# Optimization experiments

Hardware: AMD Instinct MI355X
Metric: run time of the kernel (lower is better)

## Reference

```python
import jax, jax.numpy as jnp
import numpy as np

T, B, E, H, L, V = 35, 128, 200, 512, 2, 10000


def setup_inputs() -> dict:
    key = jax.random.key(0)
    ks = jax.random.split(key, 8)
    s = 0.05  # weight init scale
    return {
        "inputs": jax.random.randint(ks[0], (T, B), 0, V),
        "hidden": jnp.zeros((L, B, H), jnp.float32),
        "emb": jax.random.normal(ks[1], (V, E), jnp.float32) * s,
        "Wx0": jax.random.normal(ks[2], (3, H, E), jnp.float32) * s,
        "Wx": jax.random.normal(ks[3], (L - 1, 3, H, H), jnp.float32) * s,
        "Wh": jax.random.normal(ks[4], (L, 3, H, H), jnp.float32) * s,
        "bh": jax.random.normal(ks[5], (L, 3, H), jnp.float32) * s,
        "Wout": jax.random.normal(ks[6], (V, H), jnp.float32) * s,
        "bout": jnp.zeros((V,), jnp.float32),
    }


def reference(inputs, hidden, emb, Wx0, Wx, Wh, bh, Wout, bout):
    # inputs: [T,B] int; hidden: [L,B,H]
    x = emb[inputs]  # [T,B,E]
    num_layers = hidden.shape[0]

    def step(h_prev, x_t):
        data = x_t  # dropout is identity (keep_prob=1.0)
        new_h = []
        for j in range(num_layers):
            Wxj = Wx0 if j == 0 else Wx[j - 1]
            gx = jnp.einsum('bi,ghi->gbh', data, Wxj)  # [3,B,H], no bias on x-side
            hp = h_prev[j]
            reset = jax.nn.sigmoid(gx[0] + hp @ Wh[j, 0].T + bh[j, 0])
            forget = jax.nn.sigmoid(gx[1] + hp @ Wh[j, 1].T + bh[j, 1])
            tild = jnp.tanh(gx[2] + (reset * hp) @ Wh[j, 2].T + bh[j, 2])
            hn = (1.0 - forget) * hp + forget * tild
            new_h.append(hn)
            data = hn  # dropout identity
        logit = data @ Wout.T + bout  # [B,V]
        return jnp.stack(new_h), logit

    h_final, logits = jax.lax.scan(step, hidden, x)
    return logits, h_final
```

## Files before the change

kernel.cpp:

```cpp
#include <hip/hip_runtime.h>
#include <hip/hip_bf16.h>

#define T_ 35
#define B_ 128
#define E_ 200
#define H_ 512
#define L_ 2
#define V_ 10000
#define BH_ (B_ * H_)
#define KPAD 224
#define NCL 4
#define CLW 48
#define NWG (NCL * CLW)

typedef __attribute__((ext_vector_type(8))) short bf16x8;
typedef __attribute__((ext_vector_type(4))) float f32x4;

__device__ __forceinline__ unsigned short f2bf(float f) {
    union { float f; unsigned u; } c; c.f = f;
    unsigned r = c.u + 0x7FFF + ((c.u >> 16) & 1);
    return (unsigned short)(r >> 16);
}
__device__ __forceinline__ float bf2f(unsigned short u) {
    union { unsigned u; float f; } c; c.u = ((unsigned)u) << 16; return c.f;
}

__device__ __forceinline__ bf16x8 cvt8(const float* src) {
    float4 w0 = *(const float4*)src;
    float4 w1 = *(const float4*)(src + 4);
    bf16x8 v;
    v[0] = (short)f2bf(w0.x); v[1] = (short)f2bf(w0.y);
    v[2] = (short)f2bf(w0.z); v[3] = (short)f2bf(w0.w);
    v[4] = (short)f2bf(w1.x); v[5] = (short)f2bf(w1.y);
    v[6] = (short)f2bf(w1.z); v[7] = (short)f2bf(w1.w);
    return v;
}

__device__ __forceinline__ void store_quad_bf16(unsigned short* buf, int idx,
                                                float v, int lane) {
    unsigned x = (unsigned)f2bf(v);
    unsigned y = (unsigned)__shfl_xor((int)x, 1);
    unsigned pair = (lane & 1) ? (y | (x << 16)) : (x | (y << 16));
    unsigned long long q = (unsigned long long)pair;
    unsigned long long p2 = (unsigned long long)(unsigned)__shfl_xor((int)pair, 2);
    unsigned long long quad = (lane & 2) ? (p2 | (q << 32)) : (q | (p2 << 32));
    if ((lane & 3) == 0)
        __hip_atomic_store((unsigned long long*)(buf + idx), quad,
                           __ATOMIC_RELAXED, __HIP_MEMORY_SCOPE_AGENT);
}

__global__ void prep_all(const float* __restrict__ emb, const float* __restrict__ Wx0,
                         const float* __restrict__ hidden, const float* __restrict__ Wout,
                         unsigned short* embB, unsigned short* wx0cat,
                         unsigned short* WoutB,
                         unsigned short* h0bt, unsigned short* h1bfx, int* flags) {
    int job = blockIdx.y;
    int stride = gridDim.x * blockDim.x;
    int i0 = blockIdx.x * blockDim.x + threadIdx.x;
    if (job == 0) {
        for (int i = i0; i < V_ * KPAD; i += stride) {
            int v = i / KPAD, k = i - v * KPAD;
            embB[i] = (k < E_) ? f2bf(emb[v * E_ + k]) : (unsigned short)0;
        }
    } else if (job == 1) {
        for (int i = i0; i < 1536 * KPAD; i += stride) {
            int n = i / KPAD, k = i - n * KPAD;
            wx0cat[i] = (k < E_) ? f2bf(Wx0[n * E_ + k]) : (unsigned short)0;
        }
    } else if (job == 2) {
        for (int i = i0; i < 2 * BH_; i += stride) {
            if (i < BH_) h0bt[i] = f2bf(hidden[i]);
            else         h1bfx[i - BH_] = f2bf(hidden[i]);
        }
        for (int i = i0; i < NWG * 32; i += stride) flags[i] = 0;
    } else {
        for (int i = i0; i < V_ * H_; i += stride) WoutB[i] = f2bf(Wout[i]);
    }
}

__global__ __launch_bounds__(256) void xside_gemm(
    const int* __restrict__ inputs, const unsigned short* __restrict__ embB,
    const unsigned short* __restrict__ wx0cat, float* __restrict__ gx0) {
    int m0 = blockIdx.x * 128, n0 = blockIdx.y * 128;
    int wave = threadIdx.x >> 6, lane = threadIdx.x & 63;
    int wr = wave >> 1, wc = wave & 1;
    int am = m0 + wr * 64, bn = n0 + wc * 64;
    int lr = lane & 15, lk = (lane >> 4) * 8;

    f32x4 acc[4][4] = {};
    int id[4];
    #pragma unroll
    for (int i = 0; i < 4; ++i) id[i] = inputs[am + i * 16 + lr];

    for (int k0 = 0; k0 < KPAD; k0 += 32) {
        bf16x8 a[4], b[4];
        #pragma unroll
        for (int i = 0; i < 4; ++i)
            a[i] = *(const bf16x8*)(embB + (size_t)id[i] * KPAD + k0 + lk);
        #pragma unroll
        for (int j = 0; j < 4; ++j)
            b[j] = *(const bf16x8*)(wx0cat + (size_t)(bn + j * 16 + lr) * KPAD + k0 + lk);
        #pragma unroll
        for (int i = 0; i < 4; ++i)
            #pragma unroll
            for (int j = 0; j < 4; ++j)
                acc[i][j] = __builtin_amdgcn_mfma_f32_16x16x32_bf16(a[i], b[j], acc[i][j], 0, 0, 0);
    }
    int crow0 = (lane >> 4) * 4, ccol = lane & 15;
    #pragma unroll
    for (int i = 0; i < 4; ++i) {
        #pragma unroll
        for (int r = 0; r < 4; ++r) {
            int row = am + i * 16 + crow0 + r;
            int t = row >> 7, b = row & 127;
            #pragma unroll
            for (int j = 0; j < 4; ++j) {
                int col = bn + j * 16 + ccol;
                int g = col >> 9, h = col & 511;
                gx0[((size_t)(t * 3 + g) * 128 + b) * 512 + h] = acc[i][j][r];
            }
        }
    }
}

__device__ __forceinline__ void bar_l0(int* flb, int wgl, int gen) {
    __syncthreads();
    if (threadIdx.x == 0)
        __hip_atomic_store(flb + wgl * 32, gen,
                           __ATOMIC_RELAXED, __HIP_MEMORY_SCOPE_AGENT);
    if (threadIdx.x < 16) {
        while (__hip_atomic_load(flb + threadIdx.x * 32, __ATOMIC_RELAXED,
                                 __HIP_MEMORY_SCOPE_AGENT) < gen)
            __builtin_amdgcn_s_sleep(1);
    }
    __syncthreads();
}

__device__ __forceinline__ void bar_l1(int* flb, int wid, int gen, int l0need) {
    __syncthreads();
    if (threadIdx.x == 0)
        __hip_atomic_store(flb + (16 + wid) * 32, gen,
                           __ATOMIC_RELAXED, __HIP_MEMORY_SCOPE_AGENT);
    if (threadIdx.x < 32) {
        while (__hip_atomic_load(flb + (16 + threadIdx.x) * 32, __ATOMIC_RELAXED,
                                 __HIP_MEMORY_SCOPE_AGENT) < gen)
            __builtin_amdgcn_s_sleep(1);
    } else if (threadIdx.x < 48) {
        while (__hip_atomic_load(flb + (threadIdx.x - 32) * 32, __ATOMIC_RELAXED,
                                 __HIP_MEMORY_SCOPE_AGENT) < l0need)
            __builtin_amdgcn_s_sleep(1);
    }
    __syncthreads();
}

__global__ __launch_bounds__(512) void scan_kernel(
    const float* __restrict__ gx0,
    const float* __restrict__ Wx, const float* __restrict__ Wh,
    const float* __restrict__ bh, const float* __restrict__ hidden,
    unsigned short* h0bt, unsigned short* rh0t, unsigned short* rh1t,
    unsigned short* h1bfx, int* flags, float* hfinal_out) {
    __shared__ unsigned short wlds[96 * 512];

    const int tid = threadIdx.x;
    const int bx = blockIdx.x;
    const int cl = bx & 3;
    const int wgl = bx >> 2;
    const int lane = tid & 63;
    const int wave = tid >> 6;
    const int lr = lane & 15;
    const int hi = lane >> 4;
    const int lk8 = hi * 8;
    const int ccol = lane & 15;
    const int crow0 = hi * 4;
    const int R0 = cl * 32;

    const bool isL0 = (wgl < 16);
    const int wid = wgl - 16;
    int* flb = flags + cl * CLW * 32;

    if (isL0) {
        for (int i = tid; i < 96 * 64; i += 512) {
            int lc = i >> 6, kg = i & 63;
            int g = lc >> 5, h = (wgl << 5) + (lc & 31);
            const float* src = Wh + (size_t)(g * 512 + h) * 512 + kg * 8;
            *(bf16x8*)(wlds + lc * 512 + (kg ^ (lc & 7)) * 8) = cvt8(src);
        }
    } else {
        for (int i = tid; i < 48 * 128; i += 512) {
            int lc = i >> 7, kg = i & 127;
            int g = lc >> 4, h = (wid << 4) + (lc & 15);
            const float* src = (kg < 64)
                ? Wx + (size_t)(g * 512 + h) * 512 + kg * 8
                : Wh + (size_t)(3 * 512 * 512) + (size_t)(g * 512 + h) * 512 + (kg - 64) * 8;
            *(bf16x8*)(wlds + lc * 1024 + (kg ^ (lc & 7)) * 8) = cvt8(src);
        }
    }

    const int mt0 = wave >> 2, nt0 = wave & 3;
    const int mt1 = (wave >> 1) & 1, nt1 = wave & 1;
    float h0reg[4], freg0[4], bias_p1_0 = 0.f, bias_p2_0 = 0.f;
    float h1reg[4], freg1[4], bias_p1_1 = 0.f, bias_p2_1 = 0.f;
    bf16x8 a0keep[16];

    if (isL0) {
        const int base = wgl << 5;
        int g = nt0 >> 1;
        int hp1 = base + (nt0 & 1) * 16 + ccol;
        bias_p1_0 = bh[g * 512 + hp1];
        if (nt0 >= 2) {
            int hc = base + (nt0 - 2) * 16 + ccol;
            int rowg = R0 + mt0 * 16;
            #pragma unroll
            for (int r = 0; r < 4; ++r)
                h0reg[r] = hidden[(size_t)(rowg + crow0 + r) * 512 + hc];
            bias_p2_0 = bh[1024 + hc];
        }
    } else {
        const int base = wid << 4;
        int hc = base + ccol;
        if (wave < 4) {
            bias_p1_1 = bh[1536 + nt1 * 512 + hc];
            if (nt1 == 1) {
                int rowg = R0 + mt1 * 16;
                #pragma unroll
                for (int r = 0; r < 4; ++r)
                    h1reg[r] = hidden[(size_t)BH_ + (size_t)(rowg + crow0 + r) * 512 + hc];
                bias_p2_1 = bh[2560 + hc];
            }
        }
    }
    __syncthreads();

    if (isL0) {
        const int base = wgl << 5;
        const int rowg = R0 + mt0 * 16;
        const int hP1 = base + (nt0 & 1) * 16 + ccol;
        const int gP1 = nt0 >> 1;
        const int ntp = (nt0 >= 2) ? (nt0 - 2) : 0;
        const int hP2 = base + ntp * 16 + ccol;

        float gxn[4];
        {
            const float* gx = gx0 + (size_t)(0 * 3 + gP1) * BH_ + hP1;
            #pragma unroll
            for (int r = 0; r < 4; ++r)
                gxn[r] = gx[(rowg + crow0 + r) * 512];
        }

        for (int s = 0; s < 2 * T_; ++s) {
            bar_l0(flb, wgl, s);
            int t = s >> 1;
            float gxc[4];
            #pragma unroll
            for (int r = 0; r < 4; ++r) gxc[r] = gxn[r];
            if (s + 1 < 2 * T_) {
                int tn = (s + 1) >> 1;
                const float* gx = (((s + 1) & 1) == 0)
                    ? gx0 + (size_t)(tn * 3 + gP1) * BH_ + hP1
                    : gx0 + (size_t)(tn * 3 + 2) * BH_ + hP2;
                #pragma unroll
                for (int r = 0; r < 4; ++r)
                    gxn[r] = gx[(rowg + crow0 + r) * 512];
            }
            if ((s & 1) == 0) {
                const unsigned short* hprev = h0bt + (size_t)t * BH_;
                unsigned short* rh0 = rh0t + (size_t)t * BH_;
                bf16x8 a[16];
                #pragma unroll
                for (int ks = 0; ks < 16; ++ks)
                    a[ks] = *(const bf16x8*)(hprev + (size_t)(rowg + lr) * 512 + ks * 32 + lk8);
                f32x4 accA = {0.f, 0.f, 0.f, 0.f}, accB = {0.f, 0.f, 0.f, 0.f};
                #pragma unroll
                for (int ks = 0; ks < 16; ks += 2) {
                    int c = nt0 * 16 + lr;
                    int kgA = 4 * ks + hi, kgB = 4 * (ks + 1) + hi;
                    bf16x8 bA = *(const bf16x8*)(wlds + c * 512 + (kgA ^ (c & 7)) * 8);
                    bf16x8 bB = *(const bf16x8*)(wlds + c * 512 + (kgB ^ (c & 7)) * 8);
                    accA = __builtin_amdgcn_mfma_f32_16x16x32_bf16(a[ks], bA, accA, 0, 0, 0);
                    accB = __builtin_amdgcn_mfma_f32_16x16x32_bf16(a[ks + 1], bB, accB, 0, 0, 0);
                }
                #pragma unroll
                for (int r = 0; r < 4; ++r) {
                    int b = rowg + crow0 + r;
                    float v = accA[r] + accB[r] + gxc[r] + bias_p1_0;
                    float sg = 1.f / (1.f + __expf(-v));
                    if (nt0 < 2) {
                        float h0p = bf2f(hprev[(size_t)b * 512 + hP1]);
                        store_quad_bf16(rh0, b * 512 + hP1 - (lane & 3), sg * h0p, lane);
                    } else {
                        freg0[r] = sg;
                    }
                }
            } else if (nt0 >= 2) {
                const unsigned short* rh0 = rh0t + (size_t)t * BH_;
                unsigned short* h0nx = h0bt + (size_t)(t + 1) * BH_;
                bf16x8 a[16];
                #pragma unroll
                for (int ks = 0; ks < 16; ++ks)
                    a[ks] = *(const bf16x8*)(rh0 + (size_t)(rowg + lr) * 512 + ks * 32 + lk8);
                f32x4 accA = {0.f, 0.f, 0.f, 0.f}, accB = {0.f, 0.f, 0.f, 0.f};
                #pragma unroll
                for (int ks = 0; ks < 16; ks += 2) {
                    int c = 64 + ntp * 16 + lr;
                    int kgA = 4 * ks + hi, kgB = 4 * (ks + 1) + hi;
                    bf16x8 bA = *(const bf16x8*)(wlds + c * 512 + (kgA ^ (c & 7)) * 8);
                    bf16x8 bB = *(const bf16x8*)(wlds + c * 512 + (kgB ^ (c & 7)) * 8);
                    accA = __builtin_amdgcn_mfma_f32_16x16x32_bf16(a[ks], bA, accA, 0, 0, 0);
                    accB = __builtin_amdgcn_mfma_f32_16x16x32_bf16(a[ks + 1], bB, accB, 0, 0, 0);
                }
                #pragma unroll
                for (int r = 0; r < 4; ++r) {
                    int b = rowg + crow0 + r;
                    float v = accA[r] + accB[r] + gxc[r] + bias_p2_0;
                    float tld = tanhf(v);
                    float hn = h0reg[r] + freg0[r] * (tld - h0reg[r]);
                    h0reg[r] = hn;
                    store_quad_bf16(h0nx, b * 512 + hP2 - (lane & 3), hn, lane);
                }
            }
        }
        __syncthreads();
        if (tid == 0)
            __hip_atomic_store(flb + wgl * 32, 2 * T_,
                               __ATOMIC_RELAXED, __HIP_MEMORY_SCOPE_AGENT);
        if (nt0 >= 2) {
            #pragma unroll
            for (int r = 0; r < 4; ++r)
                hfinal_out[(size_t)(rowg + crow0 + r) * 512 + hP2] = h0reg[r];
        }
    } else {
        for (int s = 0; s < 2 * T_; ++s) {
            int tc = s >> 1;
            int l0need = ((s & 1) == 0) ? (2 * tc + 2) : 0;
            bar_l1(flb, wid, s, l0need);
            if ((s & 1) == 0) {
                if (wave < 4) {
                    const int base = wid << 4;
                    const int rowg = R0 + mt1 * 16;
                    const unsigned short* h0cur = h0bt + (size_t)(tc + 1) * BH_;
                    const unsigned short* h1prev = h1bfx + (size_t)tc * BH_;
                    unsigned short* rh1 = rh1t + (size_t)tc * BH_;
                    bf16x8 a1[16];
                    #pragma unroll
                    for (int ks = 0; ks < 16; ++ks) {
                        a0keep[ks] = *(const bf16x8*)(h0cur + (size_t)(rowg + lr) * 512 + ks * 32 + lk8);
                        a1[ks] = *(const bf16x8*)(h1prev + (size_t)(rowg + lr) * 512 + ks * 32 + lk8);
                    }
                    f32x4 accA = {0.f, 0.f, 0.f, 0.f}, accB = {0.f, 0.f, 0.f, 0.f};
                    #pragma unroll
                    for (int ks = 0; ks < 16; ++ks) {
                        int kg = 4 * ks + hi;
                        int c = nt1 * 16 + lr;
                        bf16x8 b = *(const bf16x8*)(wlds + c * 1024 + (kg ^ (c & 7)) * 8);
                        accA = __builtin_amdgcn_mfma_f32_16x16x32_bf16(a0keep[ks], b, accA, 0, 0, 0);
                    }
                    #pragma unroll
                    for (int ks = 0; ks < 16; ++ks) {
                        int kg = 64 + 4 * ks + hi;
                        int c = nt1 * 16 + lr;
                        bf16x8 b = *(const bf16x8*)(wlds + c * 1024 + (kg ^ (c & 7)) * 8);
                        accB = __builtin_amdgcn_mfma_f32_16x16x32_bf16(a1[ks], b, accB, 0, 0, 0);
                    }
                    int h = base + ccol;
                    #pragma unroll
                    for (int r = 0; r < 4; ++r) {
                        int b = rowg + crow0 + r;
                        float v = accA[r] + accB[r] + bias_p1_1;
                        float sg = 1.f / (1.f + __expf(-v));
                        if (nt1 == 0) {
                            float h1p = bf2f(h1prev[(size_t)b * 512 + h]);
                            store_quad_bf16(rh1, b * 512 + h - (lane & 3), sg * h1p, lane);
                        } else {
                            freg1[r] = sg;
                        }
                    }
                }
            } else {
                if (wave < 4 && nt1 == 1) {
                    const int base = wid << 4;
                    const int rowg = R0 + mt1 * 16;
                    const unsigned short* rh1 = rh1t + (size_t)tc * BH_;
                    unsigned short* h1nx = h1bfx + (size_t)(tc + 1) * BH_;
                    bf16x8 a1[16];
                    #pragma unroll
                    for (int ks = 0; ks < 16; ++ks)
                        a1[ks] = *(const bf16x8*)(rh1 + (size_t)(rowg + lr) * 512 + ks * 32 + lk8);
                    f32x4 accA = {0.f, 0.f, 0.f, 0.f}, accB = {0.f, 0.f, 0.f, 0.f};
                    #pragma unroll
                    for (int ks = 0; ks < 16; ++ks) {
                        int kg = 4 * ks + hi;
                        int c = 32 + lr;
                        bf16x8 b = *(const bf16x8*)(wlds + c * 1024 + (kg ^ (c & 7)) * 8);
                        accA = __builtin_amdgcn_mfma_f32_16x16x32_bf16(a0keep[ks], b, accA, 0, 0, 0);
                    }
                    #pragma unroll
                    for (int ks = 0; ks < 16; ++ks) {
                        int kg = 64 + 4 * ks + hi;
                        int c = 32 + lr;
                        bf16x8 b = *(const bf16x8*)(wlds + c * 1024 + (kg ^ (c & 7)) * 8);
                        accB = __builtin_amdgcn_mfma_f32_16x16x32_bf16(a1[ks], b, accB, 0, 0, 0);
                    }
                    int h = base + ccol;
                    #pragma unroll
                    for (int r = 0; r < 4; ++r) {
                        int b = rowg + crow0 + r;
                        float v = accA[r] + accB[r] + bias_p2_1;
                        float tld = tanhf(v);
                        float hn = h1reg[r] + freg1[r] * (tld - h1reg[r]);
                        h1reg[r] = hn;
                        store_quad_bf16(h1nx, b * 512 + h - (lane & 3), hn, lane);
                    }
                }
            }
        }
        if (wave < 4 && nt1 == 1) {
            const int base = wid << 4;
            int rowg = R0 + mt1 * 16;
            #pragma unroll
            for (int r = 0; r < 4; ++r)
                hfinal_out[(size_t)BH_ + (size_t)(rowg + crow0 + r) * 512 + base + ccol] = h1reg[r];
        }
    }
}

#define MT_ (T_ * B_ / 128)
#define NT_ ((V_ + 127) / 128)
__global__ __launch_bounds__(256) void logits_gemm(
    const unsigned short* __restrict__ A, const unsigned short* __restrict__ Bw,
    const float* __restrict__ bout, float* __restrict__ C) {
    const int nwg = MT_ * NT_;
    const int q = nwg / 8, rr = nwg % 8;
    int bid = blockIdx.x;
    int xcd = bid % 8, idx = bid / 8;
    int wgid = (xcd < rr ? xcd * (q + 1) : rr * (q + 1) + (xcd - rr) * q) + idx;
    int n0 = (wgid / MT_) * 128;
    int m0 = (wgid % MT_) * 128;

    int wave = threadIdx.x >> 6, lane = threadIdx.x & 63;
    int wr = wave >> 1, wc = wave & 1;
    int am = m0 + wr * 64, bn = n0 + wc * 64;
    int lr = lane & 15, lk = (lane >> 4) * 8;

    f32x4 acc[4][4] = {};
    bf16x8 a[4], b[4], an[4], bnx[4];
    #pragma unroll
    for (int i = 0; i < 4; ++i)
        a[i] = *(const bf16x8*)(A + (size_t)(am + i * 16 + lr) * H_ + lk);
    #pragma unroll
    for (int j = 0; j < 4; ++j) {
        int colc = bn + j * 16 + lr; if (colc >= V_) colc = V_ - 1;
        b[j] = *(const bf16x8*)(Bw + (size_t)colc * H_ + lk);
    }
    for (int k0 = 0; k0 < H_; k0 += 32) {
        if (k0 + 32 < H_) {
            #pragma unroll
            for (int i = 0; i < 4; ++i)
                an[i] = *(const bf16x8*)(A + (size_t)(am + i * 16 + lr) * H_ + k0 + 32 + lk);
            #pragma unroll
            for (int j = 0; j < 4; ++j) {
                int colc = bn + j * 16 + lr; if (colc >= V_) colc = V_ - 1;
                bnx[j] = *(const bf16x8*)(Bw + (size_t)colc * H_ + k0 + 32 + lk);
            }
        }
        #pragma unroll
        for (int i = 0; i < 4; ++i)
            #pragma unroll
            for (int j = 0; j < 4; ++j)
                acc[i][j] = __builtin_amdgcn_mfma_f32_16x16x32_bf16(a[i], b[j], acc[i][j], 0, 0, 0);
        #pragma unroll
        for (int i = 0; i < 4; ++i) { a[i] = an[i]; b[i] = bnx[i]; }
    }
    int crow0 = (lane >> 4) * 4, ccol = lane & 15;
    #pragma unroll
    for (int j = 0; j < 4; ++j) {
        int col = bn + j * 16 + ccol;
        if (col >= V_) continue;
        float bv = bout[col];
        #pragma unroll
        for (int i = 0; i < 4; ++i) {
            #pragma unroll
            for (int r = 0; r < 4; ++r) {
                int row = am + i * 16 + crow0 + r;
                __builtin_nontemporal_store(acc[i][j][r] + bv, &C[(size_t)row * V_ + col]);
            }
        }
    }
}

extern "C" void kernel_launch(void* const* d_in, const int* in_sizes, int n_in,
                              void* d_out, int out_size, void* d_ws, size_t ws_size,
                              hipStream_t stream) {
    const int*   inputs = (const int*)  d_in[0];
    const float* hidden = (const float*)d_in[1];
    const float* emb    = (const float*)d_in[2];
    const float* Wx0    = (const float*)d_in[3];
    const float* Wx     = (const float*)d_in[4];
    const float* Wh     = (const float*)d_in[5];
    const float* bh     = (const float*)d_in[6];
    const float* Wout   = (const float*)d_in[7];
    const float* bout   = (const float*)d_in[8];
    float* out = (float*)d_out;
    (void)in_sizes; (void)n_in; (void)out_size; (void)ws_size;

    char* ws = (char*)d_ws;
    size_t off = 0;
    auto alloc = [&](size_t bytes) -> void* {
        void* p = ws + off;
        off += (bytes + 255) & ~(size_t)255;
        return p;
    };
    unsigned short* embB   = (unsigned short*)alloc((size_t)V_ * KPAD * 2);
    unsigned short* wx0cat = (unsigned short*)alloc((size_t)1536 * KPAD * 2);
    unsigned short* WoutB  = (unsigned short*)alloc((size_t)V_ * H_ * 2);
    unsigned short* h1bfx  = (unsigned short*)alloc((size_t)(T_ + 1) * BH_ * 2);
    int* flags = (int*)alloc(NWG * 32 * 4);

    float* gx0 = out;
    unsigned short* scr = (unsigned short*)(out + (size_t)T_ * 3 * BH_);
    unsigned short* h0bt = scr;
    unsigned short* rh0t = scr + (size_t)(T_ + 1) * BH_;
    unsigned short* rh1t = scr + (size_t)(2 * T_ + 1) * BH_;

    prep_all<<<dim3(1024, 4), dim3(256), 0, stream>>>(
        emb, Wx0, hidden, Wout, embB, wx0cat, WoutB, h0bt, h1bfx, flags);
    xside_gemm<<<dim3(T_, 12), dim3(256), 0, stream>>>(inputs, embB, wx0cat, gx0);
    scan_kernel<<<dim3(NWG), dim3(512), 0, stream>>>(
        gx0, Wx, Wh, bh, hidden,
        h0bt, rh0t, rh1t, h1bfx, flags,
        out + (size_t)T_ * B_ * V_);
    logits_gemm<<<dim3(MT_ * NT_), dim3(256), 0, stream>>>(
        h1bfx + BH_, WoutB, bout, out);
}
```

Measured before the change: 595.1 us.

## Fuse logits GEMM into persistent scan kernel with atomic tile queue

Merges the recurrent scan and the output-projection GEMM into one persistent launch. Extra workgroups, and the scan workgroups once they finish, pull logits tiles from an atomic queue. Each tile spin-waits on per-cluster layer-1 progress flags, so logits for a time step can start as soon as that step's hidden state exists, overlapping the GEMM with the serial scan. Tiles whose output rows alias the gx0 and scratch buffers are deferred until the scan completes. The cost is memory and compute contention on the latency-bound scan, plus smaller 128x128 tiles and extra polling.

```diff
diff --git a/kernel.cpp b/kernel.cpp
--- a/kernel.cpp
+++ b/kernel.cpp
@@ -12,6 +12,9 @@
 #define NCL 4
 #define CLW 48
 #define NWG (NCL * CLW)
+#define TOTWG 256
+#define NTL 79
+#define NTILES (T_ * NTL)
 
 typedef __attribute__((ext_vector_type(8))) short bf16x8;
 typedef __attribute__((ext_vector_type(4))) float f32x4;
@@ -72,7 +75,7 @@
             if (i < BH_) h0bt[i] = f2bf(hidden[i]);
             else         h1bfx[i - BH_] = f2bf(hidden[i]);
         }
-        for (int i = i0; i < NWG * 32; i += stride) flags[i] = 0;
+        for (int i = i0; i < NWG * 32 + 32; i += stride) flags[i] = 0;
     } else {
         for (int i = i0; i < V_ * H_; i += stride) WoutB[i] = f2bf(Wout[i]);
     }
@@ -153,18 +156,19 @@
     __syncthreads();
 }
 
-__global__ __launch_bounds__(512) void scan_kernel(
+__global__ __launch_bounds__(512) void scan_logits_kernel(
     const float* __restrict__ gx0,
     const float* __restrict__ Wx, const float* __restrict__ Wh,
     const float* __restrict__ bh, const float* __restrict__ hidden,
     unsigned short* h0bt, unsigned short* rh0t, unsigned short* rh1t,
-    unsigned short* h1bfx, int* flags, float* hfinal_out) {
+    unsigned short* h1bfx, int* flags,
+    const unsigned short* __restrict__ WoutB, const float* __restrict__ bout,
+    float* __restrict__ C, float* hfinal_out) {
     __shared__ unsigned short wlds[96 * 512];
+    __shared__ int qidx_sh;
 
     const int tid = threadIdx.x;
     const int bx = blockIdx.x;
-    const int cl = bx & 3;
-    const int wgl = bx >> 2;
     const int lane = tid & 63;
     const int wave = tid >> 6;
     const int lr = lane & 15;
@@ -172,316 +176,335 @@
     const int lk8 = hi * 8;
     const int ccol = lane & 15;
     const int crow0 = hi * 4;
-    const int R0 = cl * 32;
-
-    const bool isL0 = (wgl < 16);
-    const int wid = wgl - 16;
-    int* flb = flags + cl * CLW * 32;
-
-    if (isL0) {
-        for (int i = tid; i < 96 * 64; i += 512) {
-            int lc = i >> 6, kg = i & 63;
-            int g = lc >> 5, h = (wgl << 5) + (lc & 31);
-            const float* src = Wh + (size_t)(g * 512 + h) * 512 + kg * 8;
-            *(bf16x8*)(wlds + lc * 512 + (kg ^ (lc & 7)) * 8) = cvt8(src);
-        }
-    } else {
-        for (int i = tid; i < 48 * 128; i += 512) {
-            int lc = i >> 7, kg = i & 127;
-            int g = lc >> 4, h = (wid << 4) + (lc & 15);
-            const float* src = (kg < 64)
-                ? Wx + (size_t)(g * 512 + h) * 512 + kg * 8
-                : Wh + (size_t)(3 * 512 * 512) + (size_t)(g * 512 + h) * 512 + (kg - 64) * 8;
-            *(bf16x8*)(wlds + lc * 1024 + (kg ^ (lc & 7)) * 8) = cvt8(src);
-        }
-    }
-
-    const int mt0 = wave >> 2, nt0 = wave & 3;
-    const int mt1 = (wave >> 1) & 1, nt1 = wave & 1;
-    float h0reg[4], freg0[4], bias_p1_0 = 0.f, bias_p2_0 = 0.f;
-    float h1reg[4], freg1[4], bias_p1_1 = 0.f, bias_p2_1 = 0.f;
-    bf16x8 a0keep[16];
-
-    if (isL0) {
-        const int base = wgl << 5;
-        int g = nt0 >> 1;
-        int hp1 = base + (nt0 & 1) * 16 + ccol;
-        bias_p1_0 = bh[g * 512 + hp1];
-        if (nt0 >= 2) {
-            int hc = base + (nt0 - 2) * 16 + ccol;
-            int rowg = R0 + mt0 * 16;
-            #pragma unroll
-            for (int r = 0; r < 4; ++r)
-                h0reg[r] = hidden[(size_t)(rowg + crow0 + r) * 512 + hc];
-            bias_p2_0 = bh[1024 + hc];
-        }
-    } else {
-        const int base = wid << 4;
-        int hc = base + ccol;
-        if (wave < 4) {
-            bias_p1_1 = bh[1536 + nt1 * 512 + hc];
-            if (nt1 == 1) {
-                int rowg = R0 + mt1 * 16;
+    int* qhead = flags + NWG * 32;
+
+    if (bx < NWG) {
+        const int cl = bx & 3;
+        const int wgl = bx >> 2;
+        const int R0 = cl * 32;
+        const bool isL0 = (wgl < 16);
+        const int wid = wgl - 16;
+        int* flb = flags + cl * CLW * 32;
+
+        if (isL0) {
+            for (int i = tid; i < 96 * 64; i += 512) {
+                int lc = i >> 6, kg = i & 63;
+                int g = lc >> 5, h = (wgl << 5) + (lc & 31);
+                const float* src = Wh + (size_t)(g * 512 + h) * 512 + kg * 8;
+                *(bf16x8*)(wlds + lc * 512 + (kg ^ (lc & 7)) * 8) = cvt8(src);
+            }
+        } else {
+            for (int i = tid; i < 48 * 128; i += 512) {
+                int lc = i >> 7, kg = i & 127;
+                int g = lc >> 4, h = (wid << 4) + (lc & 15);
+                const float* src = (kg < 64)
+                    ? Wx + (size_t)(g * 512 + h) * 512 + kg * 8
+                    : Wh + (size_t)(3 * 512 * 512) + (size_t)(g * 512 + h) * 512 + (kg - 64) * 8;
+                *(bf16x8*)(wlds + lc * 1024 + (kg ^ (lc & 7)) * 8) = cvt8(src);
+            }
+        }
+
+        const int mt0 = wave >> 2, nt0 = wave & 3;
+        const int mt1 = (wave >> 1) & 1, nt1 = wave & 1;
+        float h0reg[4], freg0[4], bias_p1_0 = 0.f, bias_p2_0 = 0.f;
+        float h1reg[4], freg1[4], bias_p1_1 = 0.f, bias_p2_1 = 0.f;
+        bf16x8 a0keep[16];
+
+        if (isL0) {
+            const int base = wgl << 5;
+            int g = nt0 >> 1;
+            int hp1 = base + (nt0 & 1) * 16 + ccol;
+            bias_p1_0 = bh[g * 512 + hp1];
+            if (nt0 >= 2) {
+                int hc = base + (nt0 - 2) * 16 + ccol;
+                int rowg = R0 + mt0 * 16;
                 #pragma unroll
                 for (int r = 0; r < 4; ++r)
-                    h1reg[r] = hidden[(size_t)BH_ + (size_t)(rowg + crow0 + r) * 512 + hc];
-                bias_p2_1 = bh[2560 + hc];
-            }
-        }
-    }
-    __syncthreads();
-
-    if (isL0) {
-        const int base = wgl << 5;
-        const int rowg = R0 + mt0 * 16;
-        const int hP1 = base + (nt0 & 1) * 16 + ccol;
-        const int gP1 = nt0 >> 1;
-        const int ntp = (nt0 >= 2) ? (nt0 - 2) : 0;
-        const int hP2 = base + ntp * 16 + ccol;
-
-        float gxn[4];
-        {
-            const float* gx = gx0 + (size_t)(0 * 3 + gP1) * BH_ + hP1;
-            #pragma unroll
-            for (int r = 0; r < 4; ++r)
-                gxn[r] = gx[(rowg + crow0 + r) * 512];
-        }
-
-        for (int s = 0; s < 2 * T_; ++s) {
-            bar_l0(flb, wgl, s);
-            int t = s >> 1;
-            float gxc[4];
-            #pragma unroll
-            for (int r = 0; r < 4; ++r) gxc[r] = gxn[r];
-            if (s + 1 < 2 * T_) {
-                int tn = (s + 1) >> 1;
-                const float* gx = (((s + 1) & 1) == 0)
-                    ? gx0 + (size_t)(tn * 3 + gP1) * BH_ + hP1
-                    : gx0 + (size_t)(tn * 3 + 2) * BH_ + hP2;
+                    h0reg[r] = hidden[(size_t)(rowg + crow0 + r) * 512 + hc];
+                bias_p2_0 = bh[1024 + hc];
+            }
+        } else {
+            const int base = wid << 4;
+            int hc = base + ccol;
+            if (wave < 4) {
+                bias_p1_1 = bh[1536 + nt1 * 512 + hc];
+                if (nt1 == 1) {
+                    int rowg = R0 + mt1 * 16;
+                    #pragma unroll
+                    for (int r = 0; r < 4; ++r)
+                        h1reg[r] = hidden[(size_t)BH_ + (size_t)(rowg + crow0 + r) * 512 + hc];
+                    bias_p2_1 = bh[2560 + hc];
+                }
+            }
+        }
+        __syncthreads();
+
+        if (isL0) {
+            const int base = wgl << 5;
+            const int rowg = R0 + mt0 * 16;
+            const int hP1 = base + (nt0 & 1) * 16 + ccol;
+            const int gP1 = nt0 >> 1;
+            const int ntp = (nt0 >= 2) ? (nt0 - 2) : 0;
+            const int hP2 = base + ntp * 16 + ccol;
+
+            float gxn[4];
+            {
+                const float* gx = gx0 + (size_t)(0 * 3 + gP1) * BH_ + hP1;
                 #pragma unroll
                 for (int r = 0; r < 4; ++r)
                     gxn[r] = gx[(rowg + crow0 + r) * 512];
             }
-            if ((s & 1) == 0) {
-                const unsigned short* hprev = h0bt + (size_t)t * BH_;
-                unsigned short* rh0 = rh0t + (size_t)t * BH_;
-                bf16x8 a[16];
-                #pragma unroll
-                for (int ks = 0; ks < 16; ++ks)
-                    a[ks] = *(const bf16x8*)(hprev + (size_t)(rowg + lr) * 512 + ks * 32 + lk8);
-                f32x4 accA = {0.f, 0.f, 0.f, 0.f}, accB = {0.f, 0.f, 0.f, 0.f};
-                #pragma unroll
-                for (int ks = 0; ks < 16; ks += 2) {
-                    int c = nt0 * 16 + lr;
-                    int kgA = 4 * ks + hi, kgB = 4 * (ks + 1) + hi;
-                    bf16x8 bA = *(const bf16x8*)(wlds + c * 512 + (kgA ^ (c & 7)) * 8);
-                    bf16x8 bB = *(const bf16x8*)(wlds + c * 512 + (kgB ^ (c & 7)) * 8);
-                    accA = __builtin_amdgcn_mfma_f32_16x16x32_bf16(a[ks], bA, accA, 0, 0, 0);
-                    accB = __builtin_amdgcn_mfma_f32_16x16x32_bf16(a[ks + 1], bB, accB, 0, 0, 0);
+
+            for (int s = 0; s < 2 * T_; ++s) {
+                bar_l0(flb, wgl, s);
+                int t = s >> 1;
+                float gxc[4];
+                #pragma unroll
+                for (int r = 0; r < 4; ++r) gxc[r] = gxn[r];
+                if (s + 1 < 2 * T_) {
+                    int tn = (s + 1) >> 1;
+                    const float* gx = (((s + 1) & 1) == 0)
+                        ? gx0 + (size_t)(tn * 3 + gP1) * BH_ + hP1
+                        : gx0 + (size_t)(tn * 3 + 2) * BH_ + hP2;
+                    #pragma unroll
+                    for (int r = 0; r < 4; ++r)
+                        gxn[r] = gx[(rowg + crow0 + r) * 512];
                 }
-                #pragma unroll
-                for (int r = 0; r < 4; ++r) {
-                    int b = rowg + crow0 + r;
-                    float v = accA[r] + accB[r] + gxc[r] + bias_p1_0;
-                    float sg = 1.f / (1.f + __expf(-v));
-                    if (nt0 < 2) {
-                        float h0p = bf2f(hprev[(size_t)b * 512 + hP1]);
-                        store_quad_bf16(rh0, b * 512 + hP1 - (lane & 3), sg * h0p, lane);
-                    } else {
-                        freg0[r] = sg;
+                if ((s & 1) == 0) {
+                    const unsigned short* hprev = h0bt + (size_t)t * BH_;
+                    unsigned short* rh0 = rh0t + (size_t)t * BH_;
+                    bf16x8 a[16];
+                    #pragma unroll
+                    for (int ks = 0; ks < 16; ++ks)
+                        a[ks] = *(const bf16x8*)(hprev + (size_t)(rowg + lr) * 512 + ks * 32 + lk8);
+                    f32x4 accA = {0.f, 0.f, 0.f, 0.f}, accB = {0.f, 0.f, 0.f, 0.f};
+                    #pragma unroll
+                    for (int ks = 0; ks < 16; ks += 2) {
+                        int c = nt0 * 16 + lr;
+                        int kgA = 4 * ks + hi, kgB = 4 * (ks + 1) + hi;
+                        bf16x8 bA = *(const bf16x8*)(wlds + c * 512 + (kgA ^ (c & 7)) * 8);
+                        bf16x8 bB = *(const bf16x8*)(wlds + c * 512 + (kgB ^ (c & 7)) * 8);
+                        accA = __builtin_amdgcn_mfma_f32_16x16x32_bf16(a[ks], bA, accA, 0, 0, 0);
+                        accB = __builtin_amdgcn_mfma_f32_16x16x32_bf16(a[ks + 1], bB, accB, 0, 0, 0);
+                    }
+                    #pragma unroll
+                    for (int r = 0; r < 4; ++r) {
+                        int b = rowg + crow0 + r;
+                        float v = accA[r] + accB[r] + gxc[r] + bias_p1_0;
+                        float sg = 1.f / (1.f + __expf(-v));
+                        if (nt0 < 2) {
+                            float h0p = bf2f(hprev[(size_t)b * 512 + hP1]);
+                            store_quad_bf16(rh0, b * 512 + hP1 - (lane & 3), sg * h0p, lane);
+                        } else {
+                            freg0[r] = sg;
+                        }
+                    }
+                } else if (nt0 >= 2) {
+                    const unsigned short* rh0 = rh0t + (size_t)t * BH_;
+                    unsigned short* h0nx = h0bt + (size_t)(t + 1) * BH_;
+                    bf16x8 a[16];
+                    #pragma unroll
+                    for (int ks = 0; ks < 16; ++ks)
+                        a[ks] = *(const bf16x8*)(rh0 + (size_t)(rowg + lr) * 512 + ks * 32 + lk8);
+                    f32x4 accA = {0.f, 0.f, 0.f, 0.f}, accB = {0.f, 0.f, 0.f, 0.f};
+                    #pragma unroll
+                    for (int ks = 0; ks < 16; ks += 2) {
+                        int c = 64 + ntp * 16 + lr;
+                        int kgA = 4 * ks + hi, kgB = 4 * (ks + 1) + hi;
+                        bf16x8 bA = *(const bf16x8*)(wlds + c * 512 + (kgA ^ (c & 7)) * 8);
+                        bf16x8 bB = *(const bf16x8*)(wlds + c * 512 + (kgB ^ (c & 7)) * 8);
+                        accA = __builtin_amdgcn_mfma_f32_16x16x32_bf16(a[ks], bA, accA, 0, 0, 0);
+                        accB = __builtin_amdgcn_mfma_f32_16x16x32_bf16(a[ks + 1], bB, accB, 0, 0, 0);
+                    }
+                    #pragma unroll
+                    for (int r = 0; r < 4; ++r) {
+                        int b = rowg + crow0 + r;
+                        float v = accA[r] + accB[r] + gxc[r] + bias_p2_0;
+                        float tld = tanhf(v);
+                        float hn = h0reg[r] + freg0[r] * (tld - h0reg[r]);
+                        h0reg[r] = hn;
+                        store_quad_bf16(h0nx, b * 512 + hP2 - (lane & 3), hn, lane);
                     }
                 }
-            } else if (nt0 >= 2) {
-                const unsigned short* rh0 = rh0t + (size_t)t * BH_;
-                unsigned short* h0nx = h0bt + (size_t)(t + 1) * BH_;
-                bf16x8 a[16];
-                #pragma unroll
-                for (int ks = 0; ks < 16; ++ks)
-                    a[ks] = *(const bf16x8*)(rh0 + (size_t)(rowg + lr) * 512 + ks * 32 + lk8);
-                f32x4 accA = {0.f, 0.f, 0.f, 0.f}, accB = {0.f, 0.f, 0.f, 0.f};
-                #pragma unroll
-                for (int ks = 0; ks < 16; ks += 2) {
-                    int c = 64 + ntp * 16 + lr;
-                    int kgA = 4 * ks + hi, kgB = 4 * (ks + 1) + hi;
-                    bf16x8 bA = *(const bf16x8*)(wlds + c * 512 + (kgA ^ (c & 7)) * 8);
-                    bf16x8 bB = *(const bf16x8*)(wlds + c * 512 + (kgB ^ (c & 7)) * 8);
-                    accA = __builtin_amdgcn_mfma_f32_16x16x32_bf16(a[ks], bA, accA, 0, 0, 0);
-                    accB = __builtin_amdgcn_mfma_f32_16x16x32_bf16(a[ks + 1], bB, accB, 0, 0, 0);
-                }
-                #pragma unroll
-                for (int r = 0; r < 4; ++r) {
-                    int b = rowg + crow0 + r;
-                    float v = accA[r] + accB[r] + gxc[r] + bias_p2_0;
-                    float tld = tanhf(v);
-                    float hn = h0reg[r] + freg0[r] * (tld - h0reg[r]);
-                    h0reg[r] = hn;
-                    store_quad_bf16(h0nx, b * 512 + hP2 - (lane & 3), hn, lane);
-                }
-            }
-        }
-        __syncthreads();
-        if (tid == 0)
-            __hip_atomic_store(flb + wgl * 32, 2 * T_,
-                               __ATOMIC_RELAXED, __HIP_MEMORY_SCOPE_AGENT);
-        if (nt0 >= 2) {
-            #pragma unroll
-            for (int r = 0; r < 4; ++r)
-                hfinal_out[(size_t)(rowg + crow0 + r) * 512 + hP2] = h0reg[r];
-        }
-    } else {
-        for (int s = 0; s < 2 * T_; ++s) {
-            int tc = s >> 1;
-            int l0need = ((s & 1) == 0) ? (2 * tc + 2) : 0;
-            bar_l1(flb, wid, s, l0need);
-            if ((s & 1) == 0) {
-                if (wave < 4) {
-                    const int base = wid << 4;
-                    const int rowg = R0 + mt1 * 16;
-                    const unsigned short* h0cur = h0bt + (size_t)(tc + 1) * BH_;
-                    const unsigned short* h1prev = h1bfx + (size_t)tc * BH_;
-                    unsigned short* rh1 = rh1t + (size_t)tc * BH_;
-                    bf16x8 a1[16];
-                    #pragma unroll
-                    for (int ks = 0; ks < 16; ++ks) {
-                        a0keep[ks] = *(const bf16x8*)(h0cur + (size_t)(rowg + lr) * 512 + ks * 32 + lk8);
-                        a1[ks] = *(const bf16x8*)(h1prev + (size_t)(rowg + lr) * 512 + ks * 32 + lk8);
+            }
+            __syncthreads();
+            if (tid == 0)
+                __hip_atomic_store(flb + wgl * 32, 2 * T_,
+                                   __ATOMIC_RELAXED, __HIP_MEMORY_SCOPE_AGENT);
+            if (nt0 >= 2) {
+                #pragma unroll
+                for (int r = 0; r < 4; ++r)
+                    hfinal_out[(size_t)(rowg + crow0 + r) * 512 + hP2] = h0reg[r];
+            }
+        } else {
+            for (int s = 0; s < 2 * T_; ++s) {
+                int tc = s >> 1;
+                int l0need = ((s & 1) == 0) ? (2 * tc + 2) : 0;
+                bar_l1(flb, wid, s, l0need);
+                if ((s & 1) == 0) {
+                    if (wave < 4) {
+                        const int base = wid << 4;
+                        const int rowg = R0 + mt1 * 16;
+                        const unsigned short* h0cur = h0bt + (size_t)(tc + 1) * BH_;
+                        const unsigned short* h1prev = h1bfx + (size_t)tc * BH_;
+                        unsigned short* rh1 = rh1t + (size_t)tc * BH_;
+                        bf16x8 a1[16];
+                        #pragma unroll
+                        for (int ks = 0; ks < 16; ++ks) {
+                            a0keep[ks] = *(const bf16x8*)(h0cur + (size_t)(rowg + lr) * 512 + ks * 32 + lk8);
+                            a1[ks] = *(const bf16x8*)(h1prev + (size_t)(rowg + lr) * 512 + ks * 32 + lk8);
+                        }
+                        f32x4 accA = {0.f, 0.f, 0.f, 0.f}, accB = {0.f, 0.f, 0.f, 0.f};
+                        #pragma unroll
+                        for (int ks = 0; ks < 16; ++ks) {
+                            int kg = 4 * ks + hi;
+                            int c = nt1 * 16 + lr;
+                            bf16x8 b = *(const bf16x8*)(wlds + c * 1024 + (kg ^ (c & 7)) * 8);
+                            accA = __builtin_amdgcn_mfma_f32_16x16x32_bf16(a0keep[ks], b, accA, 0, 0, 0);
+                        }
+                        #pragma unroll
+                        for (int ks = 0; ks < 16; ++ks) {
+                            int kg = 64 + 4 * ks + hi;
+                            int c = nt1 * 16 + lr;
+                            bf16x8 b = *(const bf16x8*)(wlds + c * 1024 + (kg ^ (c & 7)) * 8);
+                            accB = __builtin_amdgcn_mfma_f32_16x16x32_bf16(a1[ks], b, accB, 0, 0, 0);
+                        }
+                        int h = base + ccol;
+                        #pragma unroll
+                        for (int r = 0; r < 4; ++r) {
+                            int b = rowg + crow0 + r;
+                            float v = accA[r] + accB[r] + bias_p1_1;
+                            float sg = 1.f / (1.f + __expf(-v));
+                            if (nt1 == 0) {
+                                float h1p = bf2f(h1prev[(size_t)b * 512 + h]);
+                                store_quad_bf16(rh1, b * 512 + h - (lane & 3), sg * h1p, lane);
+                            } else {
+                                freg1[r] = sg;
+                            }
+                        }
                     }
-                    f32x4 accA = {0.f, 0.f, 0.f, 0.f}, accB = {0.f, 0.f, 0.f, 0.f};
-                    #pragma unroll
-                    for (int ks = 0; ks < 16; ++ks) {
-                        int kg = 4 * ks + hi;
-                        int c = nt1 * 16 + lr;
-                        bf16x8 b = *(const bf16x8*)(wlds + c * 1024 + (kg ^ (c & 7)) * 8);
-                        accA = __builtin_amdgcn_mfma_f32_16x16x32_bf16(a0keep[ks], b, accA, 0, 0, 0);
-                    }
-                    #pragma unroll
-                    for (int ks = 0; ks < 16; ++ks) {
-                        int kg = 64 + 4 * ks + hi;
-                        int c = nt1 * 16 + lr;
-                        bf16x8 b = *(const bf16x8*)(wlds + c * 1024 + (kg ^ (c & 7)) * 8);
-                        accB = __builtin_amdgcn_mfma_f32_16x16x32_bf16(a1[ks], b, accB, 0, 0, 0);
-                    }
-                    int h = base + ccol;
-                    #pragma unroll
-                    for (int r = 0; r < 4; ++r) {
-                        int b = rowg + crow0 + r;
-                        float v = accA[r] + accB[r] + bias_p1_1;
-                        float sg = 1.f / (1.f + __expf(-v));
-                        if (nt1 == 0) {
-                            float h1p = bf2f(h1prev[(size_t)b * 512 + h]);
-                            store_quad_bf16(rh1, b * 512 + h - (lane & 3), sg * h1p, lane);
-                        } else {
-                            freg1[r] = sg;
+                } else {
+                    if (wave < 4 && nt1 == 1) {
+                        const int base = wid << 4;
+                        const int rowg = R0 + mt1 * 16;
+                        const unsigned short* rh1 = rh1t + (size_t)tc * BH_;
+                        unsigned short* h1nx = h1bfx + (size_t)(tc + 1) * BH_;
+                        bf16x8 a1[16];
+                        #pragma unroll
+                        for (int ks = 0; ks < 16; ++ks)
+                            a1[ks] = *(const bf16x8*)(rh1 + (size_t)(rowg + lr) * 512 + ks * 32 + lk8);
+                        f32x4 accA = {0.f, 0.f, 0.f, 0.f}, accB = {0.f, 0.f, 0.f, 0.f};
+                        #pragma unroll
+                        for (int ks = 0; ks < 16; ++ks) {
+                            int kg = 4 * ks + hi;
+                            int c = 32 + lr;
+                            bf16x8 b = *(const bf16x8*)(wlds + c * 1024 + (kg ^ (c & 7)) * 8);
+                            accA = __builtin_amdgcn_mfma_f32_16x16x32_bf16(a0keep[ks], b, accA, 0, 0, 0);
+                        }
+                        #pragma unroll
+                        for (int ks = 0; ks < 16; ++ks) {
+                            int kg = 64 + 4 * ks + hi;
+                            int c = 32 + lr;
+                            bf16x8 b = *(const bf16x8*)(wlds + c * 1024 + (kg ^ (c & 7)) * 8);
+                            accB = __builtin_amdgcn_mfma_f32_16x16x32_bf16(a1[ks], b, accB, 0, 0, 0);
+                        }
+                        int h = base + ccol;
+                        #pragma unroll
+                        for (int r = 0; r < 4; ++r) {
+                            int b = rowg + crow0 + r;
+                            float v = accA[r] + accB[r] + bias_p2_1;
+                            float tld = tanhf(v);
+                            float hn = h1reg[r] + freg1[r] * (tld - h1reg[r]);
+                            h1reg[r] = hn;
+                            store_quad_bf16(h1nx, b * 512 + h - (lane & 3), hn, lane);
                         }
                     }
                 }
-            } else {
-                if (wave < 4 && nt1 == 1) {
-                    const int base = wid << 4;
-                    const int rowg = R0 + mt1 * 16;
-                    const unsigned short* rh1 = rh1t + (size_t)tc * BH_;
-                    unsigned short* h1nx = h1bfx + (size_t)(tc + 1) * BH_;
-                    bf16x8 a1[16];
-                    #pragma unroll
-                    for (int ks = 0; ks < 16; ++ks)
-                        a1[ks] = *(const bf16x8*)(rh1 + (size_t)(rowg + lr) * 512 + ks * 32 + lk8);
-                    f32x4 accA = {0.f, 0.f, 0.f, 0.f}, accB = {0.f, 0.f, 0.f, 0.f};
-                    #pragma unroll
-                    for (int ks = 0; ks < 16; ++ks) {
-                        int kg = 4 * ks + hi;
-                        int c = 32 + lr;
-                        bf16x8 b = *(const bf16x8*)(wlds + c * 1024 + (kg ^ (c & 7)) * 8);
-                        accA = __builtin_amdgcn_mfma_f32_16x16x32_bf16(a0keep[ks], b, accA, 0, 0, 0);
-                    }
-                    #pragma unroll
-                    for (int ks = 0; ks < 16; ++ks) {
-                        int kg = 64 + 4 * ks + hi;
-                        int c = 32 + lr;
-                        bf16x8 b = *(const bf16x8*)(wlds + c * 1024 + (kg ^ (c & 7)) * 8);
-                        accB = __builtin_amdgcn_mfma_f32_16x16x32_bf16(a1[ks], b, accB, 0, 0, 0);
-                    }
-                    int h = base + ccol;
-                    #pragma unroll
-                    for (int r = 0; r < 4; ++r) {
-                        int b = rowg + crow0 + r;
-                        float v = accA[r] + accB[r] + bias_p2_1;
-                        float tld = tanhf(v);
-                        float hn = h1reg[r] + freg1[r] * (tld - h1reg[r]);
-                        h1reg[r] = hn;
-                        store_quad_bf16(h1nx, b * 512 + h - (lane & 3), hn, lane);
-                    }
+            }
+            bar_l1(flb, wid, 2 * T_, 0);
+            if (tid == 0)
+                __hip_atomic_store(flb + (16 + wid) * 32, 2 * T_ + 1,
+                                   __ATOMIC_RELAXED, __HIP_MEMORY_SCOPE_AGENT);
+            if (wave < 4 && nt1 == 1) {
+                const int base = wid << 4;
+                int rowg = R0 + mt1 * 16;
+                #pragma unroll
+                for (int r = 0; r < 4; ++r)
+                    hfinal_out[(size_t)BH_ + (size_t)(rowg + crow0 + r) * 512 + base + ccol] = h1reg[r];
+            }
+        }
+    }
+
+    const int wrL = wave >> 2;
+    const int wcL = wave & 3;
+    for (;;) {
+        if (tid == 0)
+            qidx_sh = __hip_atomic_fetch_add(qhead, 1, __ATOMIC_RELAXED,
+                                             __HIP_MEMORY_SCOPE_AGENT);
+        __syncthreads();
+        int idx = qidx_sh;
+        __syncthreads();
+        if (idx >= NTILES) break;
+        int t, n0;
+        if (idx < (T_ - 9) * NTL) { t = 9 + idx / NTL; n0 = (idx % NTL) * 128; }
+        else { int j = idx - (T_ - 9) * NTL; t = j / NTL; n0 = (j % NTL) * 128; }
+        int thr = (t >= T_ - 1 || t <= 8) ? (2 * T_ + 1) : (2 * t + 3);
+        if (tid < 4) {
+            while (__hip_atomic_load(flags + tid * CLW * 32 + 16 * 32,
+                                     __ATOMIC_RELAXED, __HIP_MEMORY_SCOPE_AGENT) < thr)
+                __builtin_amdgcn_s_sleep(2);
+        }
+        __syncthreads();
+
+        const unsigned short* A = h1bfx + (size_t)(t + 1) * BH_;
+        int am = wrL * 64, bn = n0 + wcL * 32;
+        f32x4 acc[4][2] = {};
+        bf16x8 a[4], b[2], an[4], bn2[2];
+        #pragma unroll
+        for (int i = 0; i < 4; ++i)
+            a[i] = *(const bf16x8*)(A + (size_t)(am + i * 16 + lr) * H_ + lk8 + (hi >= 2 ? 16 : 0) - (hi >= 2 ? 16 : 0));
+        #pragma unroll
+        for (int i = 0; i < 4; ++i)
+            a[i] = *(const bf16x8*)(A + (size_t)(am + i * 16 + lr) * H_ + (lane >> 4) * 8);
+        #pragma unroll
+        for (int j = 0; j < 2; ++j) {
+            int col = bn + j * 16 + lr; if (col >= V_) col = V_ - 1;
+            b[j] = *(const bf16x8*)(WoutB + (size_t)col * H_ + (lane >> 4) * 8);
+        }
+        const int lk = (lane >> 4) * 8;
+        for (int k0 = 0; k0 < H_; k0 += 32) {
+            if (k0 + 32 < H_) {
+                #pragma unroll
+                for (int i = 0; i < 4; ++i)
+                    an[i] = *(const bf16x8*)(A + (size_t)(am + i * 16 + lr) * H_ + k0 + 32 + lk);
+                #pragma unroll
+                for (int j = 0; j < 2; ++j) {
+                    int col = bn + j * 16 + lr; if (col >= V_) col = V_ - 1;
+                    bn2[j] = *(const bf16x8*)(WoutB + (size_t)col * H_ + k0 + 32 + lk);
                 }
             }
-        }
-        if (wave < 4 && nt1 == 1) {
-            const int base = wid << 4;
-            int rowg = R0 + mt1 * 16;
-            #pragma unroll
-            for (int r = 0; r < 4; ++r)
-                hfinal_out[(size_t)BH_ + (size_t)(rowg + crow0 + r) * 512 + base + ccol] = h1reg[r];
-        }
-    }
-}
-
-#define MT_ (T_ * B_ / 128)
-#define NT_ ((V_ + 127) / 128)
-__global__ __launch_bounds__(256) void logits_gemm(
-    const unsigned short* __restrict__ A, const unsigned short* __restrict__ Bw,
-    const float* __restrict__ bout, float* __restrict__ C) {
-    const int nwg = MT_ * NT_;
-    const int q = nwg / 8, rr = nwg % 8;
-    int bid = blockIdx.x;
-    int xcd = bid % 8, idx = bid / 8;
-    int wgid = (xcd < rr ? xcd * (q + 1) : rr * (q + 1) + (xcd - rr) * q) + idx;
-    int n0 = (wgid / MT_) * 128;
-    int m0 = (wgid % MT_) * 128;
-
-    int wave = threadIdx.x >> 6, lane = threadIdx.x & 63;
-    int wr = wave >> 1, wc = wave & 1;
-    int am = m0 + wr * 64, bn = n0 + wc * 64;
-    int lr = lane & 15, lk = (lane >> 4) * 8;
-
-    f32x4 acc[4][4] = {};
-    bf16x8 a[4], b[4], an[4], bnx[4];
-    #pragma unroll
-    for (int i = 0; i < 4; ++i)
-        a[i] = *(const bf16x8*)(A + (size_t)(am + i * 16 + lr) * H_ + lk);
-    #pragma unroll
-    for (int j = 0; j < 4; ++j) {
-        int colc = bn + j * 16 + lr; if (colc >= V_) colc = V_ - 1;
-        b[j] = *(const bf16x8*)(Bw + (size_t)colc * H_ + lk);
-    }
-    for (int k0 = 0; k0 < H_; k0 += 32) {
-        if (k0 + 32 < H_) {
             #pragma unroll
             for (int i = 0; i < 4; ++i)
-                an[i] = *(const bf16x8*)(A + (size_t)(am + i * 16 + lr) * H_ + k0 + 32 + lk);
+                #pragma unroll
+                for (int j = 0; j < 2; ++j)
+                    acc[i][j] = __builtin_amdgcn_mfma_f32_16x16x32_bf16(a[i], b[j], acc[i][j], 0, 0, 0);
             #pragma unroll
-            for (int j = 0; j < 4; ++j) {
-                int colc = bn + j * 16 + lr; if (colc >= V_) colc = V_ - 1;
-                bnx[j] = *(const bf16x8*)(Bw + (size_t)colc * H_ + k0 + 32 + lk);
-            }
-        }
-        #pragma unroll
-        for (int i = 0; i < 4; ++i)
+            for (int i = 0; i < 4; ++i) a[i] = an[i];
             #pragma unroll
-            for (int j = 0; j < 4; ++j)
-                acc[i][j] = __builtin_amdgcn_mfma_f32_16x16x32_bf16(a[i], b[j], acc[i][j], 0, 0, 0);
-        #pragma unroll
-        for (int i = 0; i < 4; ++i) { a[i] = an[i]; b[i] = bnx[i]; }
-    }
-    int crow0 = (lane >> 4) * 4, ccol = lane & 15;
-    #pragma unroll
-    for (int j = 0; j < 4; ++j) {
-        int col = bn + j * 16 + ccol;
-        if (col >= V_) continue;
-        float bv = bout[col];
-        #pragma unroll
-        for (int i = 0; i < 4; ++i) {
+            for (int j = 0; j < 2; ++j) b[j] = bn2[j];
+        }
+        #pragma unroll
+        for (int j = 0; j < 2; ++j) {
+            int col = bn + j * 16 + ccol;
+            if (col >= V_) continue;
+            float bv = bout[col];
             #pragma unroll
-            for (int r = 0; r < 4; ++r) {
-                int row = am + i * 16 + crow0 + r;
-                __builtin_nontemporal_store(acc[i][j][r] + bv, &C[(size_t)row * V_ + col]);
+            for (int i = 0; i < 4; ++i) {
+                #pragma unroll
+                for (int r = 0; r < 4; ++r) {
+                    int row = t * 128 + am + i * 16 + crow0 + r;
+                    __builtin_nontemporal_store(acc[i][j][r] + bv, &C[(size_t)row * V_ + col]);
+                }
             }
         }
     }
@@ -513,7 +536,7 @@
     unsigned short* wx0cat = (unsigned short*)alloc((size_t)1536 * KPAD * 2);
     unsigned short* WoutB  = (unsigned short*)alloc((size_t)V_ * H_ * 2);
     unsigned short* h1bfx  = (unsigned short*)alloc((size_t)(T_ + 1) * BH_ * 2);
-    int* flags = (int*)alloc(NWG * 32 * 4);
+    int* flags = (int*)alloc((NWG * 32 + 32) * 4);
 
     float* gx0 = out;
     unsigned short* scr = (unsigned short*)(out + (size_t)T_ * 3 * BH_);
@@ -524,10 +547,8 @@
     prep_all<<<dim3(1024, 4), dim3(256), 0, stream>>>(
         emb, Wx0, hidden, Wout, embB, wx0cat, WoutB, h0bt, h1bfx, flags);
     xside_gemm<<<dim3(T_, 12), dim3(256), 0, stream>>>(inputs, embB, wx0cat, gx0);
-    scan_kernel<<<dim3(NWG), dim3(512), 0, stream>>>(
+    scan_logits_kernel<<<dim3(TOTWG), dim3(512), 0, stream>>>(
         gx0, Wx, Wh, bh, hidden,
         h0bt, rh0t, rh1t, h1bfx, flags,
-        out + (size_t)T_ * B_ * V_);
-    logits_gemm<<<dim3(MT_ * NT_), dim3(256), 0, stream>>>(
-        h1bfx + BH_, WoutB, bout, out);
-}
+        WoutB, bout, out, out + (size_t)T_ * B_ * V_);
+}
```

New measurement: 612.9 us. 1.03x slower.
